# Optimization experiments

Hardware: AMD Instinct MI355X
Metric: run time of the kernel (lower is better)

The kernel has to match this reference:

```python
import jax, jax.numpy as jnp
import numpy as np

B, DZ, DY, DX = 2, 200, 200, 100   # batch, voxel grid
N = 200000                          # active input voxels
C_IN, C_MID, C_OUT = 16, 64, 32
K = 27                              # 3x3x3 kernel offsets
EPS = 1e-5


def _pad_per_k(kid, a_in, a_out, pad_in, pad_out):
    # pack ragged per-offset pair lists into dense [K, Pmax] with dummy padding
    counts = np.bincount(kid, minlength=K)
    P = int(counts.max())
    I = np.full((K, P), pad_in, np.int32)
    O = np.full((K, P), pad_out, np.int32)
    order = np.argsort(kid, kind='stable')
    ks = kid[order]
    starts = np.cumsum(counts) - counts
    pos = np.arange(kid.size) - starts[ks]
    I[ks, pos] = a_in[order]
    O[ks, pos] = a_out[order]
    return I, O


def _build_structure(seed=0):
    # spconv-style indice-pair generation (rulebook) in numpy
    rng = np.random.default_rng(seed)
    lin = rng.choice(B * DZ * DY * DX, size=N, replace=False)
    b, r = np.divmod(lin, DZ * DY * DX)
    z, r = np.divmod(r, DY * DX)
    y, x = np.divmod(r, DX)
    coords = np.stack([b, z, y, x], 1)
    offs = np.stack(np.meshgrid(*[np.arange(3)] * 3, indexing='ij'), -1).reshape(K, 3)
    od = np.array([(DZ - 3) // 2 + 1, (DY - 3) // 2 + 1, (DX - 3) // 2 + 1])
    # stage 1: SparseConv3d k=3 s=2 p=0 -> output site o iff i = 2*o + k
    oc = coords[:, None, 1:] - offs[None]            # (N, 27, 3)
    valid = (oc >= 0).all(-1) & (oc % 2 == 0).all(-1)
    oq = oc // 2
    valid &= (oq < od).all(-1)
    pi, pk = np.nonzero(valid)
    oz, oy, ox = oq[pi, pk, 0], oq[pi, pk, 1], oq[pi, pk, 2]
    olin = ((coords[pi, 0] * od[0] + oz) * od[1] + oy) * od[2] + ox
    uniq, inv = np.unique(olin, return_inverse=True)
    n1 = int(len(uniq))
    p1_in, p1_out = _pad_per_k(pk, pi.astype(np.int32), inv.astype(np.int32), N, n1)
    # stage 2: SubMConv3d k=3 on stage-1 sites (output sites == input sites)
    c1b, r = np.divmod(uniq, od[0] * od[1] * od[2])
    c1z, r = np.divmod(r, od[1] * od[2])
    c1y, c1x = np.divmod(r, od[2])
    coords1 = np.stack([c1b, c1z, c1y, c1x], 1)
    nc = coords1[:, None, 1:] + (offs - 1)[None]     # (n1, 27, 3) neighbor coords
    valid2 = (nc >= 0).all(-1) & (nc < od).all(-1)
    pj, pk2 = np.nonzero(valid2)
    nl = ((coords1[pj, 0] * od[0] + nc[pj, pk2, 0]) * od[1] + nc[pj, pk2, 1]) * od[2] + nc[pj, pk2, 2]
    pos = np.minimum(np.searchsorted(uniq, nl), n1 - 1)
    ok = uniq[pos] == nl
    p2_in, p2_out = _pad_per_k(pk2[ok], pos[ok].astype(np.int32), pj[ok].astype(np.int32), n1, n1)
    return p1_in, p1_out, p2_in, p2_out, n1


def _ggs(feats, W, pin, pout, n_out):
    # gather-gemm-scatter sparse conv; pin padded with feats.shape[0], pout with n_out
    fpad = jnp.concatenate([feats, jnp.zeros((1, feats.shape[1]), feats.dtype)], 0)
    out = jnp.zeros((n_out + 1, W.shape[2]), feats.dtype)
    for k in range(W.shape[0]):
        out = out.at[pout[k]].add(fpad[pin[k]] @ W[k])
    return out[:n_out]


def _bn_relu(x, g, b):
    # BatchNorm1d (training-mode batch stats, biased var) + ReLU
    m = x.mean(0)
    v = x.var(0)
    return jax.nn.relu((x - m) * jax.lax.rsqrt(v + EPS) * g + b)


def setup_inputs():
    p1_in, p1_out, p2_in, p2_out, n1 = _build_structure(0)
    key = jax.random.key(0)
    k1, k2, k3, k4 = jax.random.split(key, 4)
    return {
        'feats': jax.random.normal(k1, (N, C_IN), jnp.float32),
        'W1': jax.random.normal(k2, (K, C_IN, C_MID), jnp.float32) * 0.05,
        'gamma1': jnp.ones((C_MID,), jnp.float32),
        'beta1': jnp.zeros((C_MID,), jnp.float32),
        'W2': jax.random.normal(k3, (K, C_MID, C_MID), jnp.float32) * 0.05,
        'gamma2': jnp.ones((C_MID,), jnp.float32),
        'beta2': jnp.zeros((C_MID,), jnp.float32),
        'W3': jax.random.normal(k4, (K, C_MID, C_OUT), jnp.float32) * 0.05,
        'p1_in': jnp.asarray(p1_in), 'p1_out': jnp.asarray(p1_out),
        'p2_in': jnp.asarray(p2_in), 'p2_out': jnp.asarray(p2_out),
        'n1': n1,
    }


def reference(feats, W1, gamma1, beta1, W2, gamma2, beta2, W3, p1_in, p1_out, p2_in, p2_out, n1):
    x = _ggs(feats, W1, p1_in, p1_out, n1)                        # SparseConv3d(Cin,64,3,2)
    x = _bn_relu(x, gamma1, beta1)
    x = _bn_relu(_ggs(x, W2, p2_in, p2_out, n1), gamma2, beta2)   # SubMConv3d(64,64,3)
    return _ggs(x, W3, p1_out, p1_in, N)                          # SparseInverseConv3d: pairs swapped
```

## Files before the change

### kernel.cpp

```cpp
#include <hip/hip_runtime.h>
#include <hip/hip_bf16.h>

typedef __bf16 bf16x8 __attribute__((ext_vector_type(8)));
typedef float f32x4 __attribute__((ext_vector_type(4)));

__device__ __forceinline__ unsigned short f2bf(float x) {
  union { float f; unsigned int u; } v; v.f = x;
  unsigned int r = (v.u + 0x7FFFu + ((v.u >> 16) & 1u)) >> 16;
  return (unsigned short)r;
}
__device__ __forceinline__ float bf2f(unsigned short u) {
  union { unsigned int u; float f; } v; v.u = ((unsigned int)u) << 16;
  return v.f;
}

__global__ void cvt_feats_kernel(const float* __restrict__ f, unsigned short* __restrict__ fb, int n16) {
  int t = blockIdx.x * 256 + threadIdx.x;
  if (t >= n16) return;
  fb[t] = f2bf(f[t]);
}

__global__ void pack_w_kernel(const float* __restrict__ W, unsigned short* __restrict__ Wp,
                              int CI, int CO, int NT, int KK) {
  int t = blockIdx.x * 256 + threadIdx.x;
  int total = 27 * NT * KK * 512;
  if (t >= total) return;
  int j = t & 7, l = (t >> 3) & 63;
  int g = t >> 9;
  int kk = g % KK; g /= KK;
  int nt = g % NT; int k = g / NT;
  int kg = kk * 32 + ((l >> 4) * 8) + j;
  int c = nt * 16 + (l & 15);
  float v = (kg < CI) ? W[((size_t)k * CI + kg) * CO + c] : 0.0f;
  Wp[t] = f2bf(v);
}

__global__ void pack_w_paired_kernel(const float* __restrict__ W, unsigned short* __restrict__ Wp,
                                     int CO, int NT) {
  int t = blockIdx.x * 256 + threadIdx.x;
  int total = 14 * NT * 512;
  if (t >= total) return;
  int j = t & 7, l = (t >> 3) & 63;
  int g = t >> 9;
  int nt = g % NT; int gp = g / NT;
  int kg = ((l >> 4) * 8) + j;
  int k = 2 * gp + (kg >= 16 ? 1 : 0);
  int ci = kg & 15;
  int c = nt * 16 + (l & 15);
  float v = (k <= 26) ? W[((size_t)k * 16 + ci) * CO + c] : 0.0f;
  Wp[t] = f2bf(v);
}

__global__ void build_table_kernel(const int* __restrict__ pin, const int* __restrict__ pout,
                                   int P, int maxo, int* __restrict__ tab,
                                   const int* __restrict__ n_ptr, int n_cap) {
  int p = blockIdx.x * 256 + threadIdx.x;
  if (p >= P) return;
  int k = blockIdx.y;
  int n = n_cap;
  if (n_ptr) { int nv = n_ptr[0]; if (nv < n) n = nv; }
  size_t e = (size_t)k * P + p;
  int o = pout[e];
  if (o < n) tab[(size_t)k * maxo + o] = pin[e];
}

#define LDTAB(KC_, TARR) do {                                                    \
    int _k2 = PAIRED ? (2 * (KC_) + klb) : (KC_);                                \
    int _kc = _k2 > 26 ? 26 : _k2;                                               \
    _Pragma("unroll") for (int _m = 0; _m < MT; ++_m) {                          \
      int _t = tab[(size_t)_kc * maxo + rowm[_m]];                               \
      TARR[_m] = (PAIRED && _k2 > 26) ? -1 : _t;                                 \
    }                                                                            \
  } while (0)

#define ISSUE_A(AB, TARR, D) do {                                                \
    if (SKIP) {                                                                  \
      bool _anyv = (TARR[0] >= 0);                                               \
      _Pragma("unroll") for (int _m = 1; _m < MT; ++_m)                          \
        _anyv = _anyv || (TARR[_m] >= 0);                                        \
      D = (__ballot(_anyv) != 0ull);                                             \
    }                                                                            \
    _Pragma("unroll") for (int _m = 0; _m < MT; ++_m) {                          \
      const unsigned short* _s = Xb + (size_t)(TARR[_m] < 0 ? zrow : TARR[_m]) * ROWS + loff; \
      _Pragma("unroll") for (int kk = 0; kk < KK; ++kk)                          \
        AB[_m][kk] = *reinterpret_cast<const bf16x8*>(_s + kk * 32);             \
    }                                                                            \
  } while (0)

#define STAGE_B2(KB, PB) do {                                                    \
    _Pragma("unroll") for (int _s = 0; _s < 2; ++_s) {                           \
      if ((KB) + _s <= MAXK) {                                                   \
        size_t _kb = (size_t)((KB) + _s) * (size_t)SZ;                           \
        _Pragma("unroll") for (int _j = 0; _j < PER; ++_j) {                     \
          int _c = w * PER + _j;                                                 \
          const unsigned char* _gp = WpB + _kb + (size_t)_c * 1024 + (size_t)l * 16; \
          __builtin_amdgcn_global_load_lds(                                      \
              (const __attribute__((address_space(1))) void*)_gp,                \
              (__attribute__((address_space(3))) void*)((PB) + _s * SZ + _c * 1024), 16, 0, 0); \
        }                                                                        \
      }                                                                          \
    }                                                                            \
  } while (0)

#define STEP_CORE(BCUR, AB, D) do {                                              \
    if (!SKIP || (D)) {                                                          \
      _Pragma("unroll") for (int kk = 0; kk < KK; ++kk)                          \
        _Pragma("unroll") for (int nt = 0; nt < NT; ++nt) {                      \
          bf16x8 b = *reinterpret_cast<const bf16x8*>(&(BCUR)[(nt * KK + kk) * 1024 + l * 16]); \
          _Pragma("unroll") for (int _m = 0; _m < MT; ++_m)                      \
            acc[_m][nt] = __builtin_amdgcn_mfma_f32_16x16x32_bf16(AB[_m][kk], b, acc[_m][nt], 0, 0, 0); \
        }                                                                        \
    }                                                                            \
  } while (0)

#define GROUP_BARRIER() do {                                                     \
    __builtin_amdgcn_sched_barrier(0);                                           \
    asm volatile("s_waitcnt vmcnt(%0)" :: "n"(NWAIT) : "memory");                \
    __builtin_amdgcn_sched_barrier(0);                                           \
    __builtin_amdgcn_s_barrier();                                                \
  } while (0)

template<int KK, int NT, int MT, bool SKIP, bool PAIRED>
__global__ __launch_bounds__(256, 4) void conv_mfma_kernel(
    const unsigned short* __restrict__ Xb, const unsigned short* __restrict__ Wp,
    const int* __restrict__ tab, int maxo, int zrow,
    const int* __restrict__ n_ptr, int n_cap,
    unsigned short* __restrict__ outb, float* __restrict__ outf) {
  const int CO = NT * 16;
  const int ROWS = PAIRED ? 16 : KK * 32;
  const int RPW = 16 * MT;
  constexpr int PER = (KK * NT) / 4;
  constexpr int SZ = KK * NT * 1024;
  constexpr int MAXK = PAIRED ? 13 : 26;
  constexpr int GROUPS = PAIRED ? 6 : 13;
  constexpr int NWAIT = 2 * MT * KK + 2 * MT;

  __shared__ __align__(16) unsigned char Blds[2][2][SZ];

  int bid = blockIdx.x;
  {
    int nwg = gridDim.x;
    int q = nwg >> 3, r = nwg & 7;
    int xcd = bid & 7, orig = bid >> 3;
    bid = (xcd < r ? xcd * (q + 1) : r * (q + 1) + (xcd - r) * q) + orig;
  }

  int w = threadIdx.x >> 6, l = threadIdx.x & 63;
  int n_rows = n_cap;
  if (n_ptr) { int nv = n_ptr[0]; if (nv < n_rows) n_rows = nv; }
  if (bid * 4 * RPW >= n_rows) return;
  int lr = l & 15, lg = l >> 4;
  int klb = lg >> 1;
  int loff = PAIRED ? (lg & 1) * 8 : lg * 8;
  int wbase = bid * 4 * RPW + w * RPW;

  int rowm[MT];
#pragma unroll
  for (int m = 0; m < MT; ++m) {
    int r = wbase + m * 16 + lr;
    rowm[m] = r < n_rows ? r : (n_rows - 1);
  }

  const unsigned char* WpB = (const unsigned char*)Wp;

  f32x4 acc[MT][NT] = {};
  bf16x8 a0[MT][KK], a1[MT][KK];
  int tE[MT], tO[MT];
  bool dE = true, dO = true;

  LDTAB(0, tE);
  LDTAB(1, tO);
  STAGE_B2(0, &Blds[0][0][0]);
  __builtin_amdgcn_sched_barrier(0);
  ISSUE_A(a0, tE, dE);
  ISSUE_A(a1, tO, dO);
  LDTAB(2, tE);
  LDTAB(3, tO);
  GROUP_BARRIER();

#pragma unroll 1
  for (int g = 0; g < GROUPS; ++g) {
    int kb = g * 2;
    unsigned char* bc = &Blds[g & 1][0][0];
    unsigned char* bn = &Blds[(g + 1) & 1][0][0];
    STAGE_B2(kb + 2, bn);
    __builtin_amdgcn_sched_barrier(0);
    STEP_CORE(bc + 0 * SZ, a0, dE); ISSUE_A(a0, tE, dE); LDTAB(kb + 4, tE);
    STEP_CORE(bc + 1 * SZ, a1, dO); ISSUE_A(a1, tO, dO); LDTAB(kb + 5, tO);
    GROUP_BARRIER();
  }
  {
    unsigned char* bt = &Blds[GROUPS & 1][0][0];
    STEP_CORE(bt + 0 * SZ, a0, dE);
    if (PAIRED) STEP_CORE(bt + 1 * SZ, a1, dO);
  }

#pragma unroll
  for (int mt = 0; mt < MT; ++mt) {
    int r0 = wbase + mt * 16 + lg * 4;
#pragma unroll
    for (int rr = 0; rr < 4; ++rr) {
      int row = r0 + rr;
      if (row < n_rows) {
#pragma unroll
        for (int nt = 0; nt < NT; ++nt) {
          size_t off = (size_t)row * CO + nt * 16 + lr;
          if (outf) outf[off] = acc[mt][nt][rr];
          else outb[off] = f2bf(acc[mt][nt][rr]);
        }
      }
    }
  }
}

__global__ void bn_stats_kernel(const unsigned short* __restrict__ xb,
                                const int* __restrict__ n_ptr, int n_cap,
                                float* __restrict__ stats) {
  int c = threadIdx.x & 63, q = threadIdx.x >> 6;
  int n = n_ptr[0]; if (n > n_cap) n = n_cap;
  float s = 0.f, ss = 0.f;
  for (int r = blockIdx.x * 4 + q; r < n; r += gridDim.x * 4) {
    float v = bf2f(xb[(size_t)r * 64 + c]);
    s += v; ss += v * v;
  }
  __shared__ float ls[8][64];
  ls[q][c] = s; ls[4 + q][c] = ss;
  __syncthreads();
  if (q == 0) {
    s = ls[0][c] + ls[1][c] + ls[2][c] + ls[3][c];
    ss = ls[4][c] + ls[5][c] + ls[6][c] + ls[7][c];
    atomicAdd(&stats[c], s);
    atomicAdd(&stats[64 + c], ss);
  }
}

__global__ void bn_apply_kernel(unsigned short* __restrict__ xb,
                                const int* __restrict__ n_ptr, int n_cap,
                                const float* __restrict__ stats,
                                const float* __restrict__ gamma, const float* __restrict__ beta) {
  int c = threadIdx.x & 63, q = threadIdx.x >> 6;
  int n = n_ptr[0]; if (n > n_cap) n = n_cap;
  float inv_n = 1.f / (float)n;
  float m = stats[c] * inv_n;
  float var = stats[64 + c] * inv_n - m * m;
  float sc = gamma[c] * rsqrtf(var + 1e-5f);
  float sh = beta[c] - m * sc;
  for (int r = blockIdx.x * 4 + q; r < n; r += gridDim.x * 4) {
    size_t off = (size_t)r * 64 + c;
    float v = bf2f(xb[off]) * sc + sh;
    xb[off] = f2bf(v > 0.f ? v : 0.f);
  }
}

extern "C" void kernel_launch(void* const* d_in, const int* in_sizes, int n_in,
                              void* d_out, int out_size, void* d_ws, size_t ws_size,
                              hipStream_t stream) {
  const float* feats  = (const float*)d_in[0];
  const float* W1     = (const float*)d_in[1];
  const float* g1     = (const float*)d_in[2];
  const float* b1     = (const float*)d_in[3];
  const float* W2     = (const float*)d_in[4];
  const float* g2     = (const float*)d_in[5];
  const float* b2     = (const float*)d_in[6];
  const float* W3     = (const float*)d_in[7];
  const int* p1_in    = (const int*)d_in[8];
  const int* p1_out   = (const int*)d_in[9];
  const int* p2_in    = (const int*)d_in[10];
  const int* p2_out   = (const int*)d_in[11];
  const int* d_n1     = (const int*)d_in[12];
  float* out = (float*)d_out;

  const int N  = in_sizes[0] / 16;
  const int P1 = in_sizes[8] / 27;
  const int P2 = in_sizes[10] / 27;
  long KP1 = in_sizes[8];
  int n1b = (int)(KP1 < 980100 ? KP1 : 980100);
  int maxo = n1b > N ? n1b : N;

  char* p = (char*)d_ws;
  auto alloc = [&](size_t bytes) -> char* {
    char* r = p; p += (bytes + 255) & ~(size_t)255; return r;
  };
  unsigned short* featsb = (unsigned short*)alloc((size_t)(N + 1) * 16 * 2);
  unsigned short* x1b    = (unsigned short*)alloc((size_t)(n1b + 1) * 64 * 2);
  unsigned short* x2b    = (unsigned short*)alloc((size_t)(n1b + 1) * 64 * 2);
  unsigned short* W1p    = (unsigned short*)alloc((size_t)14 * 4 * 512 * 2);
  unsigned short* W2p    = (unsigned short*)alloc((size_t)27 * 4 * 2 * 512 * 2);
  unsigned short* W3p    = (unsigned short*)alloc((size_t)27 * 2 * 2 * 512 * 2);
  int*   tab   = (int*)alloc((size_t)maxo * 27 * 4);
  float* stats = (float*)alloc(256 * 4);
  if ((size_t)(p - (char*)d_ws) > ws_size) return;

  hipMemsetAsync(featsb + (size_t)N * 16, 0, 16 * 2, stream);
  hipMemsetAsync(x1b + (size_t)n1b * 64, 0, 64 * 2, stream);
  hipMemsetAsync(x2b + (size_t)n1b * 64, 0, 64 * 2, stream);
  hipMemsetAsync(stats, 0, 256 * 4, stream);

  cvt_feats_kernel<<<(N * 16 + 255) / 256, 256, 0, stream>>>(feats, featsb, N * 16);
  pack_w_paired_kernel<<<(14 * 4 * 512 + 255) / 256, 256, 0, stream>>>(W1, W1p, 64, 4);
  pack_w_kernel<<<(27 * 4 * 2 * 512 + 255) / 256, 256, 0, stream>>>(W2, W2p, 64, 64, 4, 2);
  pack_w_kernel<<<(27 * 2 * 2 * 512 + 255) / 256, 256, 0, stream>>>(W3, W3p, 64, 32, 2, 2);

  hipMemsetAsync(tab, 0xFF, (size_t)n1b * 27 * 4, stream);
  build_table_kernel<<<dim3((P1 + 255) / 256, 27), 256, 0, stream>>>(
      p1_in, p1_out, P1, n1b, tab, d_n1, n1b);
  conv_mfma_kernel<1, 4, 2, true, true><<<(n1b + 127) / 128, 256, 0, stream>>>(
      featsb, W1p, tab, n1b, N, d_n1, n1b, x1b, nullptr);
  bn_stats_kernel<<<1024, 256, 0, stream>>>(x1b, d_n1, n1b, stats);
  bn_apply_kernel<<<2048, 256, 0, stream>>>(x1b, d_n1, n1b, stats, g1, b1);

  hipMemsetAsync(tab, 0xFF, (size_t)n1b * 27 * 4, stream);
  build_table_kernel<<<dim3((P2 + 255) / 256, 27), 256, 0, stream>>>(
      p2_in, p2_out, P2, n1b, tab, d_n1, n1b);
  conv_mfma_kernel<2, 4, 2, false, false><<<(n1b + 127) / 128, 256, 0, stream>>>(
      x1b, W2p, tab, n1b, n1b, d_n1, n1b, x2b, nullptr);
  bn_stats_kernel<<<1024, 256, 0, stream>>>(x2b, d_n1, n1b, stats + 128);
  bn_apply_kernel<<<2048, 256, 0, stream>>>(x2b, d_n1, n1b, stats + 128, g2, b2);

  hipMemsetAsync(tab, 0xFF, (size_t)N * 27 * 4, stream);
  build_table_kernel<<<dim3((P1 + 255) / 256, 27), 256, 0, stream>>>(
      p1_out, p1_in, P1, N, tab, nullptr, N);
  conv_mfma_kernel<2, 2, 2, true, false><<<(N + 127) / 128, 256, 0, stream>>>(
      x2b, W3p, tab, N, n1b, nullptr, N, nullptr, out);
}
```

Before: 634.2 us.

## Deepen gather prefetch to four register buffers in sparse conv MFMA loop

The main loop now keeps four sets of gathered A-operand registers in flight instead of two, and each iteration processes four kernel offsets while alternating between two LDS weight buffers. The goal is to hide more global gather latency behind MFMA work. The launch-bounds occupancy hint is lowered from 4 to 3 waves per SIMD to make room for the extra registers. This trades occupancy for deeper per-wave prefetch, and the tail handling for odd step counts becomes more complex.

```diff
diff --git a/kernel.cpp b/kernel.cpp
--- a/kernel.cpp
+++ b/kernel.cpp
@@ -113,15 +113,15 @@
     }                                                                            \
   } while (0)
 
-#define GROUP_BARRIER() do {                                                     \
+#define GROUP_BARRIER(NW) do {                                                   \
     __builtin_amdgcn_sched_barrier(0);                                           \
-    asm volatile("s_waitcnt vmcnt(%0)" :: "n"(NWAIT) : "memory");                \
+    asm volatile("s_waitcnt vmcnt(%0)" :: "n"(NW) : "memory");                   \
     __builtin_amdgcn_sched_barrier(0);                                           \
     __builtin_amdgcn_s_barrier();                                                \
   } while (0)
 
 template<int KK, int NT, int MT, bool SKIP, bool PAIRED>
-__global__ __launch_bounds__(256, 4) void conv_mfma_kernel(
+__global__ __launch_bounds__(256, 3) void conv_mfma_kernel(
     const unsigned short* __restrict__ Xb, const unsigned short* __restrict__ Wp,
     const int* __restrict__ tab, int maxo, int zrow,
     const int* __restrict__ n_ptr, int n_cap,
@@ -131,9 +131,12 @@
   const int RPW = 16 * MT;
   constexpr int PER = (KK * NT) / 4;
   constexpr int SZ = KK * NT * 1024;
-  constexpr int MAXK = PAIRED ? 13 : 26;
-  constexpr int GROUPS = PAIRED ? 6 : 13;
-  constexpr int NWAIT = 2 * MT * KK + 2 * MT;
+  constexpr int NSTEP = PAIRED ? 14 : 27;
+  constexpr int MAXK = NSTEP - 1;
+  constexpr int ITERS = PAIRED ? 3 : 6;
+  constexpr int TAIL = NSTEP - 4 * ITERS;
+  constexpr int NWAIT  = 2 * MT * KK + 2 * MT;
+  constexpr int NWAIT0 = 4 * MT * KK + 4 * MT;
 
   __shared__ __align__(16) unsigned char Blds[2][2][SZ];
 
@@ -164,35 +167,49 @@
   const unsigned char* WpB = (const unsigned char*)Wp;
 
   f32x4 acc[MT][NT] = {};
-  bf16x8 a0[MT][KK], a1[MT][KK];
-  int tE[MT], tO[MT];
-  bool dE = true, dO = true;
-
-  LDTAB(0, tE);
-  LDTAB(1, tO);
-  STAGE_B2(0, &Blds[0][0][0]);
+  bf16x8 aA[MT][KK], aB[MT][KK], aC[MT][KK], aD[MT][KK];
+  int t0[MT], t1[MT], t2[MT], t3[MT];
+  bool dA = true, dB = true, dC = true, dD = true;
+
+  unsigned char* b0 = &Blds[0][0][0];
+  unsigned char* b1 = &Blds[1][0][0];
+
+  LDTAB(0, t0); LDTAB(1, t1); LDTAB(2, t2); LDTAB(3, t3);
+  asm volatile("s_waitcnt vmcnt(0)" ::: "memory");
   __builtin_amdgcn_sched_barrier(0);
-  ISSUE_A(a0, tE, dE);
-  ISSUE_A(a1, tO, dO);
-  LDTAB(2, tE);
-  LDTAB(3, tO);
-  GROUP_BARRIER();
+  STAGE_B2(0, b0);
+  __builtin_amdgcn_sched_barrier(0);
+  ISSUE_A(aA, t0, dA); ISSUE_A(aB, t1, dB);
+  ISSUE_A(aC, t2, dC); ISSUE_A(aD, t3, dD);
+  LDTAB(4, t0); LDTAB(5, t1); LDTAB(6, t2); LDTAB(7, t3);
+  GROUP_BARRIER(NWAIT0);
 
 #pragma unroll 1
-  for (int g = 0; g < GROUPS; ++g) {
-    int kb = g * 2;
-    unsigned char* bc = &Blds[g & 1][0][0];
-    unsigned char* bn = &Blds[(g + 1) & 1][0][0];
-    STAGE_B2(kb + 2, bn);
+  for (int j = 0; j < ITERS; ++j) {
+    int kb = 4 * j;
+    STAGE_B2(kb + 2, b1);
     __builtin_amdgcn_sched_barrier(0);
-    STEP_CORE(bc + 0 * SZ, a0, dE); ISSUE_A(a0, tE, dE); LDTAB(kb + 4, tE);
-    STEP_CORE(bc + 1 * SZ, a1, dO); ISSUE_A(a1, tO, dO); LDTAB(kb + 5, tO);
-    GROUP_BARRIER();
-  }
-  {
-    unsigned char* bt = &Blds[GROUPS & 1][0][0];
-    STEP_CORE(bt + 0 * SZ, a0, dE);
-    if (PAIRED) STEP_CORE(bt + 1 * SZ, a1, dO);
+    STEP_CORE(b0 + 0,  aA, dA); ISSUE_A(aA, t0, dA); LDTAB(kb + 8, t0);
+    STEP_CORE(b0 + SZ, aB, dB); ISSUE_A(aB, t1, dB); LDTAB(kb + 9, t1);
+    GROUP_BARRIER(NWAIT);
+    STAGE_B2(kb + 4, b0);
+    __builtin_amdgcn_sched_barrier(0);
+    STEP_CORE(b1 + 0,  aC, dC); ISSUE_A(aC, t2, dC); LDTAB(kb + 10, t2);
+    STEP_CORE(b1 + SZ, aD, dD); ISSUE_A(aD, t3, dD); LDTAB(kb + 11, t3);
+    GROUP_BARRIER(NWAIT);
+  }
+
+  if (TAIL == 3) {
+    STAGE_B2(4 * ITERS + 2, b1);
+  }
+  STEP_CORE(b0 + 0,  aA, dA);
+  STEP_CORE(b0 + SZ, aB, dB);
+  if (TAIL == 3) {
+    __builtin_amdgcn_sched_barrier(0);
+    asm volatile("s_waitcnt vmcnt(0)" ::: "memory");
+    __builtin_amdgcn_sched_barrier(0);
+    __builtin_amdgcn_s_barrier();
+    STEP_CORE(b1 + 0, aC, dC);
   }
 
 #pragma unroll
```

After: 641.1 us. No clear change (+1.1%).
